# Kernel tuning notes

Hardware: AMD Instinct MI355X
Metric: run time of the kernel (lower is better)

Reference implementation:

```python
import jax, jax.numpy as jnp
import numpy as np

CVOCAB = 600  # static extended-vocab size (torch code uses max(src_map)+1; src_map values < 600)


def setup_inputs() -> dict:
    key = jax.random.key(0)
    k1, k2, k3, k4, k5 = jax.random.split(key, 5)
    N, D, V = 2048, 1024, 50257  # N = batch*tlen
    B, S = 32, 400               # batch, source length
    return {
        "hidden": jax.random.normal(k1, (N, D), jnp.float32),
        "orig_prob": jax.random.normal(k2, (N, V), jnp.float32),
        "attn": jax.random.uniform(k3, (N, S), jnp.float32),
        "src_map": jax.random.randint(k4, (B, S), 0, CVOCAB, jnp.int32),
        "W_copy": jax.random.normal(k5, (1, D), jnp.float32) * 0.02,
        "b_copy": jnp.zeros((1,), jnp.float32),
    }


def reference(hidden, orig_prob, attn, src_map, W_copy, b_copy):
    batch, slen = src_map.shape
    # p_softmax over target vocab
    prob = jax.nn.softmax(orig_prob, axis=1)                  # (N, V)
    # copy switch p(z=1)
    p_copy = jax.nn.sigmoid(hidden @ W_copy.T + b_copy)       # (N, 1)
    out_prob = prob * (1.0 - p_copy)                          # (N, V)
    mul_attn = (attn * p_copy).reshape(batch, -1, slen)       # (B, T, S)

    # one-hot + bmm in the original == scatter-add of attention mass into extended vocab slots
    def scatter_batch(a, sm):
        # a: (T, S), sm: (S,) -> (T, CVOCAB), duplicates accumulate
        return jnp.zeros((a.shape[0], CVOCAB), a.dtype).at[:, sm].add(a)

    copy_prob = jax.vmap(scatter_batch)(mul_attn, src_map)    # (B, T, CVOCAB)
    return out_prob, copy_prob.reshape(-1, CVOCAB)
```

## Files before the change

### kernel.cpp

```cpp
#include <hip/hip_runtime.h>
#include <math.h>

#define WAVE 64
#define BDIM 1024
#define NIT  13
#define GRID 256

typedef float f32x4 __attribute__((ext_vector_type(4)));

__global__ __launch_bounds__(BDIM, 4) void fused_kernel(
        const float* __restrict__ x,
        const float* __restrict__ hidden,
        const float* __restrict__ W,
        const float* __restrict__ bptr,
        const float* __restrict__ attn,
        const int*   __restrict__ src_map,
        float* __restrict__ out_prob,
        float* __restrict__ copy_out,
        int N, int V, int D, int S, int C, int T) {
    const int tid  = threadIdx.x;
    const int lane = tid & (WAVE - 1);
    const int wid  = tid / WAVE;

    __shared__ float red_sum[BDIM / WAVE];
    __shared__ float red_dot[BDIM / WAVE];
    __shared__ float bcast[2];
    extern __shared__ float bins[];

    const int rpb = (N + GRID - 1) / GRID;
    const int rb  = blockIdx.x * rpb;
    const float bias = bptr[0];

    float v[NIT * 4];

    if (rb < N) {
        const float* xr = x + (size_t)rb * V;
        #pragma unroll
        for (int i = 0; i < NIT; ++i) {
            int e = (i * BDIM + tid) * 4;
            if (e + 3 < V) {
                float4 t = *(const float4*)(xr + e);
                v[4*i+0] = t.x; v[4*i+1] = t.y; v[4*i+2] = t.z; v[4*i+3] = t.w;
            } else {
                #pragma unroll
                for (int k = 0; k < 4; ++k)
                    v[4*i+k] = (e + k < V) ? xr[e + k] : -INFINITY;
            }
        }
    }

    for (int k = 0; k < rpb; ++k) {
        const int row = rb + k;
        if (row >= N) break;

        for (int j = tid; j < C; j += BDIM) bins[j] = 0.f;

        float lsum = 0.f;
        #pragma unroll
        for (int j = 0; j < NIT * 4; ++j) {
            v[j] = __expf(v[j]);
            lsum += v[j];
        }

        float ldot = 0.f;
        {
            const float* h = hidden + (size_t)row * D;
            for (int e = tid; e < D; e += BDIM)
                ldot += h[e] * W[e];
        }

        #pragma unroll
        for (int off = 32; off >= 1; off >>= 1) {
            lsum += __shfl_xor(lsum, off, WAVE);
            ldot += __shfl_xor(ldot, off, WAVE);
        }
        if (lane == 0) { red_sum[wid] = lsum; red_dot[wid] = ldot; }
        __syncthreads();
        if (tid == 0) {
            float s = 0.f, dd = 0.f;
            #pragma unroll
            for (int w = 0; w < BDIM / WAVE; ++w) { s += red_sum[w]; dd += red_dot[w]; }
            float pc = 1.f / (1.f + __expf(-(dd + bias)));
            bcast[0] = (1.f - pc) / s;
            bcast[1] = pc;
        }
        __syncthreads();
        const float scale = bcast[0];
        const float pc    = bcast[1];

        float* outr = out_prob + (size_t)row * V;
        const float* xn = x + (size_t)(row + 1) * V;
        const bool more = (k + 1 < rpb) && (row + 1 < N);
        #pragma unroll
        for (int i = 0; i < NIT; ++i) {
            int e = (i * BDIM + tid) * 4;
            if (e + 3 < V) {
                f32x4 o;
                o.x = v[4*i+0] * scale; o.y = v[4*i+1] * scale;
                o.z = v[4*i+2] * scale; o.w = v[4*i+3] * scale;
                __builtin_nontemporal_store(o, (f32x4*)(outr + e));
                if (more) {
                    float4 t = *(const float4*)(xn + e);
                    v[4*i+0] = t.x; v[4*i+1] = t.y; v[4*i+2] = t.z; v[4*i+3] = t.w;
                }
            } else {
                #pragma unroll
                for (int kk = 0; kk < 4; ++kk) {
                    if (e + kk < V) outr[e + kk] = v[4*i+kk] * scale;
                    if (more) v[4*i+kk] = (e + kk < V) ? xn[e + kk] : -INFINITY;
                }
            }
        }

        {
            const float* ar = attn + (size_t)row * S;
            const int*   sm = src_map + (size_t)(row / T) * S;
            for (int s = tid; s < S; s += BDIM)
                atomicAdd(&bins[sm[s]], ar[s] * pc);
            __syncthreads();
            float* outc = copy_out + (size_t)row * C;
            for (int j = tid; j < C; j += BDIM)
                outc[j] = bins[j];
        }
    }
}

extern "C" void kernel_launch(void* const* d_in, const int* in_sizes, int n_in,
                              void* d_out, int out_size, void* d_ws, size_t ws_size,
                              hipStream_t stream) {
    const float* hidden  = (const float*)d_in[0];
    const float* orig    = (const float*)d_in[1];
    const float* attn    = (const float*)d_in[2];
    const int*   src_map = (const int*)  d_in[3];
    const float* W       = (const float*)d_in[4];
    const float* b       = (const float*)d_in[5];

    const int D = in_sizes[4];
    const int N = in_sizes[0] / D;
    const int V = in_sizes[1] / N;
    const int S = in_sizes[2] / N;
    const int B = in_sizes[3] / S;
    const int T = N / B;
    const int C = out_size / N - V;

    float* out_prob = (float*)d_out;
    float* copy_out = (float*)d_out + (size_t)N * V;

    fused_kernel<<<GRID, BDIM, C * sizeof(float), stream>>>(
        orig, hidden, W, b, attn, src_map, out_prob, copy_out, N, V, D, S, C, T);
}
```

Before: 194.5 us.

## Pipeline next-row load with current-row store using bf16-packed exp values

Each row's exponentials are now packed as bf16 pairs, which halves their register footprint. That frees registers so the next row's fp32 values can be loaded into a separate array while the current row's outputs are still being stored. The goal is to overlap HBM reads and writes across rows without spilling. The cost is that rounding to bf16 cuts the precision of out_prob to about 3 significant digits, which may break the accuracy tolerance.

After: 340.5 us. 1.75x slower.

```diff
diff --git a/kernel.cpp b/kernel.cpp
--- a/kernel.cpp
+++ b/kernel.cpp
@@ -8,6 +8,67 @@
 
 typedef float f32x4 __attribute__((ext_vector_type(4)));
 
+__device__ __forceinline__ unsigned bf16_rne(float f) {
+    unsigned u = __float_as_uint(f);
+    return u + 0x7FFFu + ((u >> 16) & 1u);
+}
+__device__ __forceinline__ unsigned pack2(float lo, float hi) {
+    return (bf16_rne(lo) >> 16) | (bf16_rne(hi) & 0xFFFF0000u);
+}
+__device__ __forceinline__ float unpack_lo(unsigned p) { return __uint_as_float(p << 16); }
+__device__ __forceinline__ float unpack_hi(unsigned p) { return __uint_as_float(p & 0xFFFF0000u); }
+
+__device__ __forceinline__ void load_row(const float* __restrict__ xr, int tid, int V,
+                                         float* f) {
+    #pragma unroll
+    for (int i = 0; i < NIT; ++i) {
+        int e = (i * BDIM + tid) * 4;
+        if (e + 3 < V) {
+            float4 t = *(const float4*)(xr + e);
+            f[4*i+0] = t.x; f[4*i+1] = t.y; f[4*i+2] = t.z; f[4*i+3] = t.w;
+        } else {
+            #pragma unroll
+            for (int k = 0; k < 4; ++k)
+                f[4*i+k] = (e + k < V) ? xr[e + k] : -INFINITY;
+        }
+    }
+}
+
+__device__ __forceinline__ float exp_pack(const float* f, unsigned* pk) {
+    float s = 0.f;
+    #pragma unroll
+    for (int i = 0; i < 2 * NIT; ++i) {
+        float a = __expf(f[2*i]);
+        float b = __expf(f[2*i+1]);
+        s += a + b;
+        pk[i] = pack2(a, b);
+    }
+    return s;
+}
+
+__device__ __forceinline__ void store_row(float* __restrict__ outr, const unsigned* pk,
+                                          float scale, int tid, int V) {
+    #pragma unroll
+    for (int i = 0; i < NIT; ++i) {
+        int e = (i * BDIM + tid) * 4;
+        if (e + 3 < V) {
+            f32x4 o;
+            o.x = unpack_lo(pk[2*i])   * scale;
+            o.y = unpack_hi(pk[2*i])   * scale;
+            o.z = unpack_lo(pk[2*i+1]) * scale;
+            o.w = unpack_hi(pk[2*i+1]) * scale;
+            __builtin_nontemporal_store(o, (f32x4*)(outr + e));
+        } else {
+            #pragma unroll
+            for (int k = 0; k < 4; ++k) {
+                float val = (k & 1) ? unpack_hi(pk[2*i + (k >> 1)])
+                                    : unpack_lo(pk[2*i + (k >> 1)]);
+                if (e + k < V) outr[e + k] = val * scale;
+            }
+        }
+    }
+}
+
 __global__ __launch_bounds__(BDIM, 4) void fused_kernel(
         const float* __restrict__ x,
         const float* __restrict__ hidden,
@@ -17,7 +78,7 @@
         const int*   __restrict__ src_map,
         float* __restrict__ out_prob,
         float* __restrict__ copy_out,
-        int N, int V, int D, int S, int C, int T) {
+        int N, int V, int D, int S, int C, int T, int rpb) {
     const int tid  = threadIdx.x;
     const int lane = tid & (WAVE - 1);
     const int wid  = tid / WAVE;
@@ -27,48 +88,22 @@
     __shared__ float bcast[2];
     extern __shared__ float bins[];
 
-    const int rpb = (N + GRID - 1) / GRID;
-    const int rb  = blockIdx.x * rpb;
+    const int rb = blockIdx.x * rpb;
+    if (rb >= N) return;
     const float bias = bptr[0];
 
-    float v[NIT * 4];
+    float    f[NIT * 4];
+    unsigned pk[NIT * 2];
+    float scale, pc;
 
-    if (rb < N) {
-        const float* xr = x + (size_t)rb * V;
-        #pragma unroll
-        for (int i = 0; i < NIT; ++i) {
-            int e = (i * BDIM + tid) * 4;
-            if (e + 3 < V) {
-                float4 t = *(const float4*)(xr + e);
-                v[4*i+0] = t.x; v[4*i+1] = t.y; v[4*i+2] = t.z; v[4*i+3] = t.w;
-            } else {
-                #pragma unroll
-                for (int k = 0; k < 4; ++k)
-                    v[4*i+k] = (e + k < V) ? xr[e + k] : -INFINITY;
-            }
-        }
-    }
+    for (int j = tid; j < C; j += BDIM) bins[j] = 0.f;
 
-    for (int k = 0; k < rpb; ++k) {
-        const int row = rb + k;
-        if (row >= N) break;
-
-        for (int j = tid; j < C; j += BDIM) bins[j] = 0.f;
-
-        float lsum = 0.f;
-        #pragma unroll
-        for (int j = 0; j < NIT * 4; ++j) {
-            v[j] = __expf(v[j]);
-            lsum += v[j];
-        }
-
+    {
+        load_row(x + (size_t)rb * V, tid, V, f);
+        float lsum = exp_pack(f, pk);
         float ldot = 0.f;
-        {
-            const float* h = hidden + (size_t)row * D;
-            for (int e = tid; e < D; e += BDIM)
-                ldot += h[e] * W[e];
-        }
-
+        const float* h = hidden + (size_t)rb * D;
+        for (int e = tid; e < D; e += BDIM) ldot += h[e] * W[e];
         #pragma unroll
         for (int off = 32; off >= 1; off >>= 1) {
             lsum += __shfl_xor(lsum, off, WAVE);
@@ -80,37 +115,22 @@
             float s = 0.f, dd = 0.f;
             #pragma unroll
             for (int w = 0; w < BDIM / WAVE; ++w) { s += red_sum[w]; dd += red_dot[w]; }
-            float pc = 1.f / (1.f + __expf(-(dd + bias)));
-            bcast[0] = (1.f - pc) / s;
-            bcast[1] = pc;
+            float p = 1.f / (1.f + __expf(-(dd + bias)));
+            bcast[0] = (1.f - p) / s;
+            bcast[1] = p;
         }
         __syncthreads();
-        const float scale = bcast[0];
-        const float pc    = bcast[1];
+        scale = bcast[0]; pc = bcast[1];
+    }
 
-        float* outr = out_prob + (size_t)row * V;
-        const float* xn = x + (size_t)(row + 1) * V;
+    for (int k = 0; k < rpb; ++k) {
+        const int row  = rb + k;
+        if (row >= N) break;
         const bool more = (k + 1 < rpb) && (row + 1 < N);
-        #pragma unroll
-        for (int i = 0; i < NIT; ++i) {
-            int e = (i * BDIM + tid) * 4;
-            if (e + 3 < V) {
-                f32x4 o;
-                o.x = v[4*i+0] * scale; o.y = v[4*i+1] * scale;
-                o.z = v[4*i+2] * scale; o.w = v[4*i+3] * scale;
-                __builtin_nontemporal_store(o, (f32x4*)(outr + e));
-                if (more) {
-                    float4 t = *(const float4*)(xn + e);
-                    v[4*i+0] = t.x; v[4*i+1] = t.y; v[4*i+2] = t.z; v[4*i+3] = t.w;
-                }
-            } else {
-                #pragma unroll
-                for (int kk = 0; kk < 4; ++kk) {
-                    if (e + kk < V) outr[e + kk] = v[4*i+kk] * scale;
-                    if (more) v[4*i+kk] = (e + kk < V) ? xn[e + kk] : -INFINITY;
-                }
-            }
-        }
+
+        if (more) load_row(x + (size_t)(row + 1) * V, tid, V, f);
+
+        store_row(out_prob + (size_t)row * V, pk, scale, tid, V);
 
         {
             const float* ar = attn + (size_t)row * S;
@@ -119,8 +139,34 @@
                 atomicAdd(&bins[sm[s]], ar[s] * pc);
             __syncthreads();
             float* outc = copy_out + (size_t)row * C;
-            for (int j = tid; j < C; j += BDIM)
+            for (int j = tid; j < C; j += BDIM) {
                 outc[j] = bins[j];
+                bins[j] = 0.f;
+            }
+        }
+
+        if (more) {
+            float lsum = exp_pack(f, pk);
+            float ldot = 0.f;
+            const float* h = hidden + (size_t)(row + 1) * D;
+            for (int e = tid; e < D; e += BDIM) ldot += h[e] * W[e];
+            #pragma unroll
+            for (int off = 32; off >= 1; off >>= 1) {
+                lsum += __shfl_xor(lsum, off, WAVE);
+                ldot += __shfl_xor(ldot, off, WAVE);
+            }
+            if (lane == 0) { red_sum[wid] = lsum; red_dot[wid] = ldot; }
+            __syncthreads();
+            if (tid == 0) {
+                float s = 0.f, dd = 0.f;
+                #pragma unroll
+                for (int w = 0; w < BDIM / WAVE; ++w) { s += red_sum[w]; dd += red_dot[w]; }
+                float p = 1.f / (1.f + __expf(-(dd + bias)));
+                bcast[0] = (1.f - p) / s;
+                bcast[1] = p;
+            }
+            __syncthreads();
+            scale = bcast[0]; pc = bcast[1];
         }
     }
 }
@@ -142,10 +188,12 @@
     const int B = in_sizes[3] / S;
     const int T = N / B;
     const int C = out_size / N - V;
+    const int rpb = (N + GRID - 1) / GRID;
 
     float* out_prob = (float*)d_out;
     float* copy_out = (float*)d_out + (size_t)N * V;
 
     fused_kernel<<<GRID, BDIM, C * sizeof(float), stream>>>(
-        orig, hidden, W, b, attn, src_map, out_prob, copy_out, N, V, D, S, C, T);
+        orig, hidden, W, b, attn, src_map, out_prob, copy_out,
+        N, V, D, S, C, T, rpb);
 }
```
